# Kernel optimization log

Hardware: AMD Instinct MI355X
Metric: run time of the kernel (lower is better)

## Reference

```python
import jax, jax.numpy as jnp
import numpy as np

B, L, D, DIN, A, V, R = 1024, 100, 256, 704, 128, 32000, 129


def setup_inputs() -> dict:
    key = jax.random.key(0)
    ks = jax.random.split(key, 18)
    s = 0.05
    inp = {
        "x": jax.random.normal(ks[0], (B, DIN), jnp.float32),
        "h0": jax.random.normal(ks[1], (B, D), jnp.float32),
        "c0": jax.random.normal(ks[2], (B, D), jnp.float32),
        "src_enc": jax.random.normal(ks[3], (B, L, D), jnp.float32),
        "src_token_ids": jax.random.randint(ks[4], (B, L), 0, V),
        "W_ih": jax.random.normal(ks[5], (4 * D, DIN), jnp.float32) * s,
        "b_ih": jax.random.normal(ks[6], (4 * D,), jnp.float32) * s,
        "W_hh": jax.random.normal(ks[7], (4 * D, D), jnp.float32) * s,
        "b_hh": jax.random.normal(ks[8], (4 * D,), jnp.float32) * s,
        "W_attn": jax.random.normal(ks[9], (D, D), jnp.float32) * s,
        "W_att_vec": jax.random.normal(ks[10], (A * 2, 2 * D), jnp.float32) * s,
        "W_ptr": jax.random.normal(ks[11], (D, D), jnp.float32) * s,
        "rule_emb": jax.random.normal(ks[12], (R, 128), jnp.float32) * s,
        "W_rule_proj": jax.random.normal(ks[13], (D, 128), jnp.float32) * s,
        "prim_emb": jax.random.normal(ks[14], (V, 128), jnp.float32) * s,
        "W_prim_proj": jax.random.normal(ks[15], (D, 128), jnp.float32) * s,
        "w_gen": jax.random.normal(ks[16], (2, D), jnp.float32) * s,
        "b_gen": jax.random.normal(ks[17], (2,), jnp.float32) * s,
    }
    # W_att_vec maps concat(h, ctx) [2D] -> ATT (=256); keep shape (256, 512)
    inp["W_att_vec"] = inp["W_att_vec"][:256]
    return inp


def reference(x, h0, c0, src_enc, src_token_ids, W_ih, b_ih, W_hh, b_hh,
              W_attn, W_att_vec, W_ptr, rule_emb, W_rule_proj,
              prim_emb, W_prim_proj, w_gen, b_gen):
    # --- LSTMCell (torch gate order i, f, g, o) ---
    gates = x @ W_ih.T + b_ih + h0 @ W_hh.T + b_hh          # [B, 4D]
    i, f, g, o = jnp.split(gates, 4, axis=-1)
    i, f, o = jax.nn.sigmoid(i), jax.nn.sigmoid(f), jax.nn.sigmoid(o)
    c = f * c0 + i * jnp.tanh(g)
    h = o * jnp.tanh(c)                                      # [B, D]

    # --- dot-product attention over source encodings ---
    enc_proj = src_enc @ W_attn.T                            # [B, L, D]
    scores = jnp.einsum('bd,bld->bl', h, enc_proj)
    alpha = jax.nn.softmax(scores, axis=-1)
    ctx = jnp.einsum('bl,bld->bd', alpha, src_enc)
    att = jnp.tanh(jnp.concatenate([h, ctx], axis=-1) @ W_att_vec.T)  # [B, 256]

    # --- apply-rule (production) readout ---
    rule_proj = rule_emb @ W_rule_proj.T                     # [R, 256]
    log_p_rule = jax.nn.log_softmax(att @ rule_proj.T, axis=-1)  # [B, R]

    # --- primitive generation readout ---
    prim_proj = prim_emb @ W_prim_proj.T                     # [V, 256]
    p_gen_prim = jax.nn.softmax(att @ prim_proj.T, axis=-1)  # [B, V]

    # --- pointer network copy distribution over source positions ---
    ptr_scores = jnp.einsum('bld,bd->bl', src_enc @ W_ptr.T, att)
    copy_p = jax.nn.softmax(ptr_scores, axis=-1)             # [B, L]

    # --- gen vs copy gate (softmax over 2, per usage in parse()) ---
    gate = jax.nn.softmax(att @ w_gen.T + b_gen, axis=-1)    # [B, 2]

    # --- combined primitive distribution: gen + scattered copy mass ---
    p_prim = gate[:, :1] * p_gen_prim                        # [B, V]
    copy_mass = gate[:, 1:] * copy_p                         # [B, L]
    bidx = jnp.arange(p_prim.shape[0])[:, None]
    p_prim = p_prim.at[bidx, src_token_ids].add(copy_mass)
    return log_p_rule, p_prim, h, c, att
```

## Files before the change

kernel.cpp:

```cpp
#include <hip/hip_runtime.h>
#include <hip/hip_bf16.h>
#include <math.h>

#define NB   1024
#define LL   100
#define DD   256
#define DINN 704
#define VV   32000
#define RR   129
#define KAV  512
#define ROWU 129

typedef float f32x4 __attribute__((ext_vector_type(4)));
typedef float f32x2 __attribute__((ext_vector_type(2)));
typedef short s16x8 __attribute__((ext_vector_type(8)));
typedef unsigned short u16;
typedef unsigned int u32;

__device__ __forceinline__ float sigf(float x) { return 1.0f / (1.0f + __expf(-x)); }

__device__ __forceinline__ u16 f2bf(float f) {
    u32 u = __float_as_uint(f);
    u += 0x7fffu + ((u >> 16) & 1u);
    return (u16)(u >> 16);
}
__device__ __forceinline__ float bf2f(u16 s) {
    return __uint_as_float(((u32)s) << 16);
}

__global__ __launch_bounds__(256, 2) void k_lstm(
    const float* __restrict__ x, const float* __restrict__ h0, const float* __restrict__ c0,
    const float* __restrict__ W_ih, const float* __restrict__ b_ih,
    const float* __restrict__ W_hh, const float* __restrict__ b_hh,
    float* __restrict__ out_h, float* __restrict__ out_c)
{
    __shared__ __align__(16) float As[16][36];
    __shared__ __align__(16) float Bs[16][68];
    __shared__ __align__(16) float gsm[32][68];
    const int t = threadIdx.x;
    const int row0 = blockIdx.x * 32;
    const int dg = blockIdx.y;
    const int tr = t >> 4, tc = t & 15;
    float acc[2][4] = {};

    for (int kt = 0; kt < 60; ++kt) {
        const float* __restrict__ Asrc;
        const float* __restrict__ Bsrc;
        int lda, kb;
        if (kt < 44) { Asrc = x;  Bsrc = W_ih; lda = DINN; kb = kt * 16; }
        else         { Asrc = h0; Bsrc = W_hh; lda = DD;   kb = (kt - 44) * 16; }
        __syncthreads();
#pragma unroll
        for (int p = 0; p < 2; ++p) {
            int e = t + p * 256;
            int r = e >> 4, kk = e & 15;
            As[kk][r] = Asrc[(row0 + r) * lda + kb + kk];
        }
#pragma unroll
        for (int p = 0; p < 4; ++p) {
            int e = t + p * 256;
            int r = e >> 4, kk = e & 15;
            int n = ((r >> 4) << 8) + dg * 16 + (r & 15);
            Bs[kk][r] = Bsrc[n * lda + kb + kk];
        }
        __syncthreads();
#pragma unroll
        for (int kk = 0; kk < 16; ++kk) {
            float a0 = As[kk][tr * 2], a1 = As[kk][tr * 2 + 1];
            f32x4 b = *reinterpret_cast<const f32x4*>(&Bs[kk][tc * 4]);
#pragma unroll
            for (int i = 0; i < 4; ++i) {
                acc[0][i] = fmaf(a0, b[i], acc[0][i]);
                acc[1][i] = fmaf(a1, b[i], acc[1][i]);
            }
        }
    }
    __syncthreads();
#pragma unroll
    for (int j = 0; j < 2; ++j)
#pragma unroll
        for (int i = 0; i < 4; ++i)
            gsm[tr * 2 + j][tc * 4 + i] = acc[j][i];
    __syncthreads();

#pragma unroll
    for (int p = 0; p < 2; ++p) {
        int item = t + p * 256;
        int r = item >> 4, di = item & 15;
        int dcol = dg * 16 + di;
        float iv = gsm[r][di]      + b_ih[dcol]          + b_hh[dcol];
        float fv = gsm[r][16 + di] + b_ih[DD + dcol]     + b_hh[DD + dcol];
        float gv = gsm[r][32 + di] + b_ih[2 * DD + dcol] + b_hh[2 * DD + dcol];
        float ov = gsm[r][48 + di] + b_ih[3 * DD + dcol] + b_hh[3 * DD + dcol];
        float cprev = c0[(row0 + r) * DD + dcol];
        float cc = sigf(fv) * cprev + sigf(iv) * tanhf(gv);
        float hh = sigf(ov) * tanhf(cc);
        out_c[(row0 + r) * DD + dcol] = cc;
        out_h[(row0 + r) * DD + dcol] = hh;
    }
}

__global__ __launch_bounds__(256) void k_conv(
    const float* __restrict__ src, u16* __restrict__ dst,
    const float* __restrict__ rule_emb, const float* __restrict__ W_rule_proj,
    float* __restrict__ rpT)
{
    __shared__ float re_s[128];
    const int bx = blockIdx.x, t = threadIdx.x;

    if (bx < RR && t < 128) re_s[t] = rule_emb[bx * 128 + t];

    int i = (bx * 256 + t) * 8;
    f32x4 a = *reinterpret_cast<const f32x4*>(&src[i]);
    f32x4 b = *reinterpret_cast<const f32x4*>(&src[i + 4]);
    s16x8 r;
    r[0] = (short)f2bf(a[0]); r[1] = (short)f2bf(a[1]);
    r[2] = (short)f2bf(a[2]); r[3] = (short)f2bf(a[3]);
    r[4] = (short)f2bf(b[0]); r[5] = (short)f2bf(b[1]);
    r[6] = (short)f2bf(b[2]); r[7] = (short)f2bf(b[3]);
    *reinterpret_cast<s16x8*>(&dst[i]) = r;

    if (bx < RR) {
        __syncthreads();
        float acc = 0.f;
        const float* __restrict__ wr = &W_rule_proj[t * 128];
#pragma unroll 8
        for (int k = 0; k < 128; k += 4) {
            f32x4 w4 = *reinterpret_cast<const f32x4*>(&wr[k]);
            acc += w4[0] * re_s[k] + w4[1] * re_s[k + 1]
                 + w4[2] * re_s[k + 2] + w4[3] * re_s[k + 3];
        }
        rpT[t * 192 + bx] = acc;
    }
}

__global__ __launch_bounds__(256) void k_hw(
    const float* __restrict__ h, const float* __restrict__ W_attn, float* __restrict__ hW)
{
    __shared__ __align__(16) float As[16][36];
    __shared__ __align__(16) float Bs[16][68];
    const int t = threadIdx.x;
    const int row0 = blockIdx.x * 32;
    const int col0 = blockIdx.y * 64;
    const int tr = t >> 4, tc = t & 15;
    float acc[2][4] = {};
    for (int kt = 0; kt < 16; ++kt) {
        __syncthreads();
#pragma unroll
        for (int p = 0; p < 2; ++p) {
            int e = t + p * 256;
            int r = e >> 4, kk = e & 15;
            As[kk][r] = h[(row0 + r) * DD + kt * 16 + kk];
        }
#pragma unroll
        for (int p = 0; p < 4; ++p) {
            int e = t + p * 256;
            int kk = e >> 6, c = e & 63;
            Bs[kk][c] = W_attn[(kt * 16 + kk) * DD + col0 + c];
        }
        __syncthreads();
#pragma unroll
        for (int kk = 0; kk < 16; ++kk) {
            float a0 = As[kk][tr * 2], a1 = As[kk][tr * 2 + 1];
            f32x4 b = *reinterpret_cast<const f32x4*>(&Bs[kk][tc * 4]);
#pragma unroll
            for (int i = 0; i < 4; ++i) {
                acc[0][i] = fmaf(a0, b[i], acc[0][i]);
                acc[1][i] = fmaf(a1, b[i], acc[1][i]);
            }
        }
    }
#pragma unroll
    for (int j = 0; j < 2; ++j) {
        f32x4 v;
#pragma unroll
        for (int i = 0; i < 4; ++i) v[i] = acc[j][i];
        *reinterpret_cast<f32x4*>(&hW[(row0 + tr * 2 + j) * DD + col0 + tc * 4]) = v;
    }
}

__global__ __launch_bounds__(256, 2) void k_attn2(
    const float* __restrict__ src_enc, const float* __restrict__ hW,
    float* __restrict__ ctx_out)
{
    __shared__ u32 enc_u[LL * ROWU];
    __shared__ __align__(16) float part[4][DD];
    __shared__ __align__(16) float hw_s[DD];
    __shared__ float sc_s[LL];
    __shared__ float al_s[LL];

    const int b = blockIdx.x, t = threadIdx.x;
    const int lane = t & 63, w = t >> 6;
    const float* __restrict__ enc = src_enc + (size_t)b * LL * DD;

    hw_s[t] = hW[b * DD + t];

#pragma unroll
    for (int p = 0; p < 25; ++p) {
        int q = p * 256 + t;
        int l = q >> 6, dq = q & 63;
        f32x4 ev = *reinterpret_cast<const f32x4*>(&enc[l * DD + dq * 4]);
        u32 w0 = (u32)f2bf(ev[0]) | ((u32)f2bf(ev[1]) << 16);
        u32 w1 = (u32)f2bf(ev[2]) | ((u32)f2bf(ev[3]) << 16);
        enc_u[l * ROWU + dq * 2]     = w0;
        enc_u[l * ROWU + dq * 2 + 1] = w1;
    }
    __syncthreads();

    {
        const int sl = ((w >> 1) << 6) + lane;
        float sp = 0.f;
        if (sl < LL) {
            const u32* __restrict__ rp = enc_u + sl * ROWU + ((w & 1) << 6);
            const float* __restrict__ hp = hw_s + ((w & 1) << 7);
#pragma unroll 32
            for (int k = 0; k < 64; ++k) {
                u32 v = rp[k];
                sp = fmaf(bf2f((u16)v),         hp[2 * k],     sp);
                sp = fmaf(bf2f((u16)(v >> 16)), hp[2 * k + 1], sp);
            }
        }
        part[w][lane] = sp;
    }
    __syncthreads();
    if (t < LL) sc_s[t] = part[(t >> 6) << 1][t & 63] + part[((t >> 6) << 1) + 1][t & 63];
    __syncthreads();

    if (w == 0) {
        float v0 = sc_s[lane];
        float v1 = (lane + 64 < LL) ? sc_s[lane + 64] : -1e30f;
        float m = fmaxf(v0, v1);
#pragma unroll
        for (int s = 1; s < 64; s <<= 1) m = fmaxf(m, __shfl_xor(m, s));
        float e0 = __expf(v0 - m);
        float e1 = (lane + 64 < LL) ? __expf(v1 - m) : 0.f;
        float ssum = e0 + e1;
#pragma unroll
        for (int s = 1; s < 64; s <<= 1) ssum += __shfl_xor(ssum, s);
        float inv = 1.f / ssum;
        al_s[lane] = e0 * inv;
        if (lane + 64 < LL) al_s[lane + 64] = e1 * inv;
    }
    __syncthreads();

    {
        const int l0 = w * 25;
        float c0 = 0.f, c1 = 0.f, c2 = 0.f, c3 = 0.f;
#pragma unroll
        for (int li = 0; li < 25; ++li) {
            int l = l0 + li;
            float a = al_s[l];
            u32 v0 = enc_u[l * ROWU + lane * 2];
            u32 v1 = enc_u[l * ROWU + lane * 2 + 1];
            c0 = fmaf(a, bf2f((u16)v0), c0);
            c1 = fmaf(a, bf2f((u16)(v0 >> 16)), c1);
            c2 = fmaf(a, bf2f((u16)v1), c2);
            c3 = fmaf(a, bf2f((u16)(v1 >> 16)), c3);
        }
        f32x4 p; p[0] = c0; p[1] = c1; p[2] = c2; p[3] = c3;
        *reinterpret_cast<f32x4*>(&part[w][lane * 4]) = p;
    }
    __syncthreads();
    ctx_out[b * DD + t] = (part[0][t] + part[1][t]) + (part[2][t] + part[3][t]);
}

__global__ __launch_bounds__(256) void k_att(
    const float* __restrict__ h, const float* __restrict__ ctx,
    const float* __restrict__ W_att_vec, float* __restrict__ att_out)
{
    __shared__ __align__(16) float As[16][36];
    __shared__ __align__(16) float Bs[16][68];
    const int t = threadIdx.x;
    const int row0 = blockIdx.x * 32;
    const int col0 = blockIdx.y * 64;
    const int tr = t >> 4, tc = t & 15;
    float acc[2][4] = {};
    for (int kt = 0; kt < 32; ++kt) {
        const float* __restrict__ Asrc = (kt < 16) ? h : ctx;
        int kb = (kt < 16) ? kt * 16 : (kt - 16) * 16;
        int kg = kt * 16;
        __syncthreads();
#pragma unroll
        for (int p = 0; p < 2; ++p) {
            int e = t + p * 256;
            int r = e >> 4, kk = e & 15;
            As[kk][r] = Asrc[(row0 + r) * DD + kb + kk];
        }
#pragma unroll
        for (int p = 0; p < 4; ++p) {
            int e = t + p * 256;
            int r = e >> 4, kk = e & 15;
            Bs[kk][r] = W_att_vec[(col0 + r) * KAV + kg + kk];
        }
        __syncthreads();
#pragma unroll
        for (int kk = 0; kk < 16; ++kk) {
            float a0 = As[kk][tr * 2], a1 = As[kk][tr * 2 + 1];
            f32x4 b = *reinterpret_cast<const f32x4*>(&Bs[kk][tc * 4]);
#pragma unroll
            for (int i = 0; i < 4; ++i) {
                acc[0][i] = fmaf(a0, b[i], acc[0][i]);
                acc[1][i] = fmaf(a1, b[i], acc[1][i]);
            }
        }
    }
#pragma unroll
    for (int j = 0; j < 2; ++j)
#pragma unroll
        for (int i = 0; i < 4; ++i)
            att_out[(row0 + tr * 2 + j) * DD + col0 + tc * 4 + i] = tanhf(acc[j][i]);
}

__global__ __launch_bounds__(256) void k_ptrproj(
    const float* __restrict__ att, const float* __restrict__ W_ptr,
    const float* __restrict__ W_prim_proj, const float* __restrict__ rpT,
    float* __restrict__ atw, u16* __restrict__ att_bf, float* __restrict__ rl)
{
    __shared__ __align__(16) float As[16][36];
    __shared__ __align__(16) float Bs[16][68];
    const int t = threadIdx.x;
    const int row0 = blockIdx.x * 32;
    const int col0 = blockIdx.y * 64;
    const int tr = t >> 4, tc = t & 15;
    float acc[2][4] = {};
    for (int kt = 0; kt < 16; ++kt) {
        __syncthreads();
#pragma unroll
        for (int p = 0; p < 2; ++p) {
            int e = t + p * 256;
            int r = e >> 4, kk = e & 15;
            As[kk][r] = att[(row0 + r) * DD + kt * 16 + kk];
        }
#pragma unroll
        for (int p = 0; p < 4; ++p) {
            int e = t + p * 256;
            int kk = e >> 6, c = e & 63;
            float bv;
            if (col0 < 256)      bv = W_ptr[(kt * 16 + kk) * DD + col0 + c];
            else if (col0 < 384) bv = W_prim_proj[(kt * 16 + kk) * 128 + (col0 - 256) + c];
            else {
                int rc = col0 - 384 + c;
                bv = (rc < RR) ? rpT[(kt * 16 + kk) * 192 + rc] : 0.f;
            }
            Bs[kk][c] = bv;
        }
        __syncthreads();
#pragma unroll
        for (int kk = 0; kk < 16; ++kk) {
            float a0 = As[kk][tr * 2], a1 = As[kk][tr * 2 + 1];
            f32x4 b = *reinterpret_cast<const f32x4*>(&Bs[kk][tc * 4]);
#pragma unroll
            for (int i = 0; i < 4; ++i) {
                acc[0][i] = fmaf(a0, b[i], acc[0][i]);
                acc[1][i] = fmaf(a1, b[i], acc[1][i]);
            }
        }
    }
    if (col0 < 256) {
#pragma unroll
        for (int j = 0; j < 2; ++j) {
            f32x4 v;
#pragma unroll
            for (int i = 0; i < 4; ++i) v[i] = acc[j][i];
            *reinterpret_cast<f32x4*>(&atw[(row0 + tr * 2 + j) * DD + col0 + tc * 4]) = v;
        }
    } else if (col0 < 384) {
#pragma unroll
        for (int j = 0; j < 2; ++j)
#pragma unroll
            for (int i = 0; i < 4; ++i)
                att_bf[(row0 + tr * 2 + j) * 128 + (col0 - 256) + tc * 4 + i] = f2bf(acc[j][i]);
    } else {
#pragma unroll
        for (int j = 0; j < 2; ++j)
#pragma unroll
            for (int i = 0; i < 4; ++i) {
                int rc = col0 - 384 + tc * 4 + i;
                if (rc < RR) rl[(row0 + tr * 2 + j) * 132 + rc] = acc[j][i];
            }
    }
}

__global__ __launch_bounds__(256) void k_fin(
    const float* __restrict__ rl, const float* __restrict__ att,
    const float* __restrict__ w_gen, const float* __restrict__ b_gen,
    float* __restrict__ log_p_rule, float* __restrict__ gate0_ws,
    float* __restrict__ gate1_ws)
{
    const int w = threadIdx.x >> 6, lane = threadIdx.x & 63;
    const int b = blockIdx.x * 4 + w;

    float v0 = rl[b * 132 + lane];
    float v1 = rl[b * 132 + 64 + lane];
    float v2 = (lane == 0) ? rl[b * 132 + 128] : -1e30f;
    float m = fmaxf(fmaxf(v0, v1), v2);
#pragma unroll
    for (int s = 1; s < 64; s <<= 1) m = fmaxf(m, __shfl_xor(m, s));
    float ssum = __expf(v0 - m) + __expf(v1 - m) + ((lane == 0) ? __expf(v2 - m) : 0.f);
#pragma unroll
    for (int s = 1; s < 64; s <<= 1) ssum += __shfl_xor(ssum, s);
    float ls = m + logf(ssum);
    log_p_rule[b * RR + lane] = v0 - ls;
    log_p_rule[b * RR + 64 + lane] = v1 - ls;
    if (lane == 0) log_p_rule[b * RR + 128] = v2 - ls;

    f32x4 a4 = *reinterpret_cast<const f32x4*>(&att[b * DD + lane * 4]);
    f32x4 g0 = *reinterpret_cast<const f32x4*>(&w_gen[lane * 4]);
    f32x4 g1 = *reinterpret_cast<const f32x4*>(&w_gen[DD + lane * 4]);
    float p0 = a4[0] * g0[0] + a4[1] * g0[1] + a4[2] * g0[2] + a4[3] * g0[3];
    float p1 = a4[0] * g1[0] + a4[1] * g1[1] + a4[2] * g1[2] + a4[3] * g1[3];
#pragma unroll
    for (int s = 1; s < 64; s <<= 1) { p0 += __shfl_xor(p0, s); p1 += __shfl_xor(p1, s); }
    if (lane == 0) {
        float ga = p0 + b_gen[0], gb = p1 + b_gen[1];
        float gm = fmaxf(ga, gb);
        float ea = __expf(ga - gm), eb = __expf(gb - gm);
        gate0_ws[b] = ea / (ea + eb);
        gate1_ws[b] = eb / (ea + eb);
    }
}

__global__ __launch_bounds__(256, 4) void k_ptr2(
    const float* __restrict__ src_enc, const float* __restrict__ atw,
    const float* __restrict__ gate1_ws, float* __restrict__ copy_mass)
{
    __shared__ __align__(16) float aw_s[DD];
    __shared__ float sc_s[LL];
    const int b = blockIdx.x, t = threadIdx.x;
    const int lane = t & 63, w = t >> 6;

    aw_s[t] = atw[b * DD + t];
    __syncthreads();

    if (t < LL) {
        const float* __restrict__ er = src_enc + (size_t)b * LL * DD + t * DD;
        float a0 = 0.f, a1 = 0.f, a2 = 0.f, a3 = 0.f;
#pragma unroll 16
        for (int d = 0; d < 64; ++d) {
            f32x4 ev = *reinterpret_cast<const f32x4*>(&er[d * 4]);
            f32x4 av = *reinterpret_cast<const f32x4*>(&aw_s[d * 4]);
            a0 = fmaf(ev[0], av[0], a0);
            a1 = fmaf(ev[1], av[1], a1);
            a2 = fmaf(ev[2], av[2], a2);
            a3 = fmaf(ev[3], av[3], a3);
        }
        sc_s[t] = (a0 + a1) + (a2 + a3);
    }
    __syncthreads();

    if (w == 0) {
        float gate1 = gate1_ws[b];
        float v0 = sc_s[lane];
        float v1 = (lane + 64 < LL) ? sc_s[lane + 64] : -1e30f;
        float m = fmaxf(v0, v1);
#pragma unroll
        for (int s = 1; s < 64; s <<= 1) m = fmaxf(m, __shfl_xor(m, s));
        float ee0 = __expf(v0 - m);
        float ee1 = (lane + 64 < LL) ? __expf(v1 - m) : 0.f;
        float ssum = ee0 + ee1;
#pragma unroll
        for (int s = 1; s < 64; s <<= 1) ssum += __shfl_xor(ssum, s);
        float inv = 1.f / ssum;
        copy_mass[b * LL + lane] = gate1 * ee0 * inv;
        if (lane + 64 < LL) copy_mass[b * LL + lane + 64] = gate1 * ee1 * inv;
    }
}

template <int PASS>
__global__ __launch_bounds__(256) void k_prim(
    const u16* __restrict__ att_bf, const u16* __restrict__ prim_bf,
    const float* __restrict__ coef, float* __restrict__ stats, float* __restrict__ p_prim)
{
    const int t = threadIdx.x;
    const int lane = t & 63, w = t >> 6;
    const int lm = lane & 15, lq = lane >> 4;
    const int colbase = blockIdx.x * 128 + (w & 1) * 64;
    const int chunk = colbase >> 6;
    const int rowblk = blockIdx.y * 256;

    s16x8 pfr[4][4];
#pragma unroll
    for (int kg = 0; kg < 4; ++kg)
#pragma unroll
        for (int mg = 0; mg < 4; ++mg)
            pfr[kg][mg] = *reinterpret_cast<const s16x8*>(
                &prim_bf[(size_t)(colbase + mg * 16 + lm) * 128 + kg * 32 + lq * 8]);

    for (int it = 0; it < 2; ++it) {
        const int rowbase = rowblk + it * 128 + (w >> 1) * 64;
        f32x4 acc[4][4] = {};
#pragma unroll
        for (int kg = 0; kg < 4; ++kg) {
            s16x8 afr[4];
#pragma unroll
            for (int ng = 0; ng < 4; ++ng)
                afr[ng] = *reinterpret_cast<const s16x8*>(
                    &att_bf[(rowbase + ng * 16 + lm) * 128 + kg * 32 + lq * 8]);
#pragma unroll
            for (int mg = 0; mg < 4; ++mg)
#pragma unroll
                for (int ng = 0; ng < 4; ++ng)
                    acc[mg][ng] = __builtin_amdgcn_mfma_f32_16x16x32_bf16(
                        pfr[kg][mg], afr[ng], acc[mg][ng], 0, 0, 0);
        }
        if (PASS == 0) {
#pragma unroll
            for (int ng = 0; ng < 4; ++ng) {
                float se = 0.f;
#pragma unroll
                for (int mg = 0; mg < 4; ++mg)
                    se += __expf(acc[mg][ng][0]) + __expf(acc[mg][ng][1])
                        + __expf(acc[mg][ng][2]) + __expf(acc[mg][ng][3]);
                se += __shfl_xor(se, 16);
                se += __shfl_xor(se, 32);
                if (lq == 0)
                    stats[chunk * NB + rowbase + ng * 16 + lm] = se;
            }
        } else {
#pragma unroll
            for (int ng = 0; ng < 4; ++ng) {
                const int arow = rowbase + ng * 16 + lm;
                const float cf = coef[arow];
                float* __restrict__ dst = &p_prim[(size_t)arow * VV + colbase + lq * 4];
#pragma unroll
                for (int mg = 0; mg < 4; ++mg) {
                    f32x4 v;
                    v[0] = cf * __expf(acc[mg][ng][0]);
                    v[1] = cf * __expf(acc[mg][ng][1]);
                    v[2] = cf * __expf(acc[mg][ng][2]);
                    v[3] = cf * __expf(acc[mg][ng][3]);
                    *reinterpret_cast<f32x4*>(&dst[mg * 16]) = v;
                }
            }
        }
    }
}

__global__ __launch_bounds__(256) void k_combine(
    const float* __restrict__ stats, const float* __restrict__ gate0_ws,
    float* __restrict__ coef)
{
    const int row = blockIdx.x * 256 + threadIdx.x;
    float s0 = 0.f, s1 = 0.f, s2 = 0.f, s3 = 0.f;
    for (int c = 0; c < 500; c += 4) {
        s0 += stats[(c)     * NB + row];
        s1 += stats[(c + 1) * NB + row];
        s2 += stats[(c + 2) * NB + row];
        s3 += stats[(c + 3) * NB + row];
    }
    coef[row] = gate0_ws[row] / ((s0 + s1) + (s2 + s3));
}

__global__ __launch_bounds__(256) void k_scatter(
    const int* __restrict__ tok, const float* __restrict__ copy_mass, float* __restrict__ p_prim)
{
    int i = blockIdx.x * 256 + threadIdx.x;
    if (i >= NB * LL) return;
    int b = i / LL;
    atomicAdd(&p_prim[(size_t)b * VV + tok[i]], copy_mass[i]);
}

extern "C" void kernel_launch(void* const* d_in, const int* in_sizes, int n_in,
                              void* d_out, int out_size, void* d_ws, size_t ws_size,
                              hipStream_t stream)
{
    const float* x         = (const float*)d_in[0];
    const float* h0        = (const float*)d_in[1];
    const float* c0        = (const float*)d_in[2];
    const float* src_enc   = (const float*)d_in[3];
    const int*   tok       = (const int*)  d_in[4];
    const float* W_ih      = (const float*)d_in[5];
    const float* b_ih      = (const float*)d_in[6];
    const float* W_hh      = (const float*)d_in[7];
    const float* b_hh      = (const float*)d_in[8];
    const float* W_attn    = (const float*)d_in[9];
    const float* W_att_vec = (const float*)d_in[10];
    const float* W_ptr     = (const float*)d_in[11];
    const float* rule_emb  = (const float*)d_in[12];
    const float* W_rule_pr = (const float*)d_in[13];
    const float* prim_emb  = (const float*)d_in[14];
    const float* W_prim_pr = (const float*)d_in[15];
    const float* w_gen     = (const float*)d_in[16];
    const float* b_gen     = (const float*)d_in[17];

    float* out    = (float*)d_out;
    float* o_logp = out;
    float* o_pp   = out + 1024 * 129;
    float* o_h    = o_pp + (size_t)1024 * 32000;
    float* o_c    = o_h + 1024 * 256;
    float* o_att  = o_c + 1024 * 256;

    float* wsf      = (float*)d_ws;
    float* ws_rpT   = wsf;
    float* ws_rl    = ws_rpT   + 49152;
    float* ws_gate0 = ws_rl    + 135168;
    float* ws_gate1 = ws_gate0 + 1024;
    float* ws_cm    = ws_gate1 + 1024;
    float* ws_coef  = ws_cm    + 102400;
    float* ws_hw    = ws_coef  + 1024;
    float* ws_ctx   = ws_hw    + 262144;
    float* ws_atw   = ws_ctx   + 262144;
    float* ws_stats = ws_atw   + 262144;
    u16*   ws_attbf = (u16*)(ws_stats + 512000);
    u16*   ws_primbf= (u16*)(ws_stats + 512000 + 65536);

    k_conv<<<dim3(2000), 256, 0, stream>>>(prim_emb, ws_primbf, rule_emb, W_rule_pr, ws_rpT);
    k_lstm<<<dim3(32, 16), 256, 0, stream>>>(x, h0, c0, W_ih, b_ih, W_hh, b_hh, o_h, o_c);
    k_hw<<<dim3(32, 4), 256, 0, stream>>>(o_h, W_attn, ws_hw);
    k_attn2<<<dim3(1024), 256, 0, stream>>>(src_enc, ws_hw, ws_ctx);
    k_att<<<dim3(32, 4), 256, 0, stream>>>(o_h, ws_ctx, W_att_vec, o_att);
    k_ptrproj<<<dim3(32, 9), 256, 0, stream>>>(o_att, W_ptr, W_prim_pr, ws_rpT,
                                               ws_atw, ws_attbf, ws_rl);
    k_fin<<<dim3(256), 256, 0, stream>>>(ws_rl, o_att, w_gen, b_gen,
                                         o_logp, ws_gate0, ws_gate1);
    k_ptr2<<<dim3(1024), 256, 0, stream>>>(src_enc, ws_atw, ws_gate1, ws_cm);
    k_prim<0><<<dim3(250, 4), 256, 0, stream>>>(ws_attbf, ws_primbf, nullptr, ws_stats, nullptr);
    k_combine<<<dim3(4), 256, 0, stream>>>(ws_stats, ws_gate0, ws_coef);
    k_prim<1><<<dim3(250, 4), 256, 0, stream>>>(ws_attbf, ws_primbf, ws_coef, nullptr, o_pp);
    k_scatter<<<dim3(400), 256, 0, stream>>>(tok, ws_cm, o_pp);
}
```

Measured before the change: 257.7 us.

## Convert LSTM gate GEMM to bf16 MFMA and warp-reduce pointer scores

The LSTM gate GEMM moves from fp32 FMA tiling with shared memory onto bf16 MFMA 16x16x32 instructions. Fragments are loaded directly from bf16 copies of x, h0, W_ih and W_hh, which the existing conversion kernel now produces as extra blocks. Separately, the pointer-score kernel now computes each dot product with a whole wave and shuffle reduction, replacing one thread per source row, to get coalesced src_enc reads. The price is bf16 precision in the gate pre-activations plus extra conversion traffic and workspace.

```diff
diff --git a/kernel.cpp b/kernel.cpp
--- a/kernel.cpp
+++ b/kernel.cpp
@@ -28,89 +28,28 @@
     return __uint_as_float(((u32)s) << 16);
 }
 
-__global__ __launch_bounds__(256, 2) void k_lstm(
-    const float* __restrict__ x, const float* __restrict__ h0, const float* __restrict__ c0,
-    const float* __restrict__ W_ih, const float* __restrict__ b_ih,
-    const float* __restrict__ W_hh, const float* __restrict__ b_hh,
-    float* __restrict__ out_h, float* __restrict__ out_c)
-{
-    __shared__ __align__(16) float As[16][36];
-    __shared__ __align__(16) float Bs[16][68];
-    __shared__ __align__(16) float gsm[32][68];
-    const int t = threadIdx.x;
-    const int row0 = blockIdx.x * 32;
-    const int dg = blockIdx.y;
-    const int tr = t >> 4, tc = t & 15;
-    float acc[2][4] = {};
-
-    for (int kt = 0; kt < 60; ++kt) {
-        const float* __restrict__ Asrc;
-        const float* __restrict__ Bsrc;
-        int lda, kb;
-        if (kt < 44) { Asrc = x;  Bsrc = W_ih; lda = DINN; kb = kt * 16; }
-        else         { Asrc = h0; Bsrc = W_hh; lda = DD;   kb = (kt - 44) * 16; }
-        __syncthreads();
-#pragma unroll
-        for (int p = 0; p < 2; ++p) {
-            int e = t + p * 256;
-            int r = e >> 4, kk = e & 15;
-            As[kk][r] = Asrc[(row0 + r) * lda + kb + kk];
-        }
-#pragma unroll
-        for (int p = 0; p < 4; ++p) {
-            int e = t + p * 256;
-            int r = e >> 4, kk = e & 15;
-            int n = ((r >> 4) << 8) + dg * 16 + (r & 15);
-            Bs[kk][r] = Bsrc[n * lda + kb + kk];
-        }
-        __syncthreads();
-#pragma unroll
-        for (int kk = 0; kk < 16; ++kk) {
-            float a0 = As[kk][tr * 2], a1 = As[kk][tr * 2 + 1];
-            f32x4 b = *reinterpret_cast<const f32x4*>(&Bs[kk][tc * 4]);
-#pragma unroll
-            for (int i = 0; i < 4; ++i) {
-                acc[0][i] = fmaf(a0, b[i], acc[0][i]);
-                acc[1][i] = fmaf(a1, b[i], acc[1][i]);
-            }
-        }
-    }
-    __syncthreads();
-#pragma unroll
-    for (int j = 0; j < 2; ++j)
-#pragma unroll
-        for (int i = 0; i < 4; ++i)
-            gsm[tr * 2 + j][tc * 4 + i] = acc[j][i];
-    __syncthreads();
-
-#pragma unroll
-    for (int p = 0; p < 2; ++p) {
-        int item = t + p * 256;
-        int r = item >> 4, di = item & 15;
-        int dcol = dg * 16 + di;
-        float iv = gsm[r][di]      + b_ih[dcol]          + b_hh[dcol];
-        float fv = gsm[r][16 + di] + b_ih[DD + dcol]     + b_hh[DD + dcol];
-        float gv = gsm[r][32 + di] + b_ih[2 * DD + dcol] + b_hh[2 * DD + dcol];
-        float ov = gsm[r][48 + di] + b_ih[3 * DD + dcol] + b_hh[3 * DD + dcol];
-        float cprev = c0[(row0 + r) * DD + dcol];
-        float cc = sigf(fv) * cprev + sigf(iv) * tanhf(gv);
-        float hh = sigf(ov) * tanhf(cc);
-        out_c[(row0 + r) * DD + dcol] = cc;
-        out_h[(row0 + r) * DD + dcol] = hh;
-    }
-}
-
 __global__ __launch_bounds__(256) void k_conv(
-    const float* __restrict__ src, u16* __restrict__ dst,
+    const float* __restrict__ prim_emb, u16* __restrict__ prim_bf,
+    const float* __restrict__ W_ih, u16* __restrict__ wih_bf,
+    const float* __restrict__ W_hh, u16* __restrict__ whh_bf,
+    const float* __restrict__ x, u16* __restrict__ x_bf,
+    const float* __restrict__ h0, u16* __restrict__ h0_bf,
     const float* __restrict__ rule_emb, const float* __restrict__ W_rule_proj,
     float* __restrict__ rpT)
 {
     __shared__ float re_s[128];
     const int bx = blockIdx.x, t = threadIdx.x;
 
+    const float* src; u16* dst; int off;
+    if (bx < 2000)      { src = prim_emb; dst = prim_bf; off = bx * 2048; }
+    else if (bx < 2352) { src = W_ih;  dst = wih_bf; off = (bx - 2000) * 2048; }
+    else if (bx < 2480) { src = W_hh;  dst = whh_bf; off = (bx - 2352) * 2048; }
+    else if (bx < 2832) { src = x;     dst = x_bf;   off = (bx - 2480) * 2048; }
+    else                { src = h0;    dst = h0_bf;  off = (bx - 2832) * 2048; }
+
     if (bx < RR && t < 128) re_s[t] = rule_emb[bx * 128 + t];
 
-    int i = (bx * 256 + t) * 8;
+    int i = off + t * 8;
     f32x4 a = *reinterpret_cast<const f32x4*>(&src[i]);
     f32x4 b = *reinterpret_cast<const f32x4*>(&src[i + 4]);
     s16x8 r;
@@ -131,6 +70,86 @@
                  + w4[2] * re_s[k + 2] + w4[3] * re_s[k + 3];
         }
         rpT[t * 192 + bx] = acc;
+    }
+}
+
+__global__ __launch_bounds__(256) void k_lstm(
+    const u16* __restrict__ x_bf, const u16* __restrict__ h0_bf,
+    const float* __restrict__ c0,
+    const u16* __restrict__ wih_bf, const u16* __restrict__ whh_bf,
+    const float* __restrict__ b_ih, const float* __restrict__ b_hh,
+    float* __restrict__ out_h, float* __restrict__ out_c)
+{
+    const int t = threadIdx.x;
+    const int lane = t & 63, w = t >> 6;
+    const int lm = lane & 15, lq = lane >> 4;
+    const int dg = blockIdx.x;
+    const int row0 = blockIdx.y * 128 + w * 32;
+    f32x4 acc[4][2] = {};
+
+    for (int kt = 0; kt < 22; ++kt) {
+        const int ko = kt * 32 + lq * 8;
+        s16x8 bfr[4], afr[2];
+#pragma unroll
+        for (int mg = 0; mg < 4; ++mg)
+            bfr[mg] = *reinterpret_cast<const s16x8*>(
+                &wih_bf[(mg * 256 + dg * 16 + lm) * DINN + ko]);
+#pragma unroll
+        for (int ng = 0; ng < 2; ++ng)
+            afr[ng] = *reinterpret_cast<const s16x8*>(
+                &x_bf[(row0 + ng * 16 + lm) * DINN + ko]);
+#pragma unroll
+        for (int mg = 0; mg < 4; ++mg)
+#pragma unroll
+            for (int ng = 0; ng < 2; ++ng)
+                acc[mg][ng] = __builtin_amdgcn_mfma_f32_16x16x32_bf16(
+                    bfr[mg], afr[ng], acc[mg][ng], 0, 0, 0);
+    }
+    for (int kt = 0; kt < 8; ++kt) {
+        const int ko = kt * 32 + lq * 8;
+        s16x8 bfr[4], afr[2];
+#pragma unroll
+        for (int mg = 0; mg < 4; ++mg)
+            bfr[mg] = *reinterpret_cast<const s16x8*>(
+                &whh_bf[(mg * 256 + dg * 16 + lm) * DD + ko]);
+#pragma unroll
+        for (int ng = 0; ng < 2; ++ng)
+            afr[ng] = *reinterpret_cast<const s16x8*>(
+                &h0_bf[(row0 + ng * 16 + lm) * DD + ko]);
+#pragma unroll
+        for (int mg = 0; mg < 4; ++mg)
+#pragma unroll
+            for (int ng = 0; ng < 2; ++ng)
+                acc[mg][ng] = __builtin_amdgcn_mfma_f32_16x16x32_bf16(
+                    bfr[mg], afr[ng], acc[mg][ng], 0, 0, 0);
+    }
+
+    const int dc = dg * 16 + lq * 4;
+    f32x4 bi[4];
+#pragma unroll
+    for (int mg = 0; mg < 4; ++mg) {
+        f32x4 a4 = *reinterpret_cast<const f32x4*>(&b_ih[mg * 256 + dc]);
+        f32x4 b4 = *reinterpret_cast<const f32x4*>(&b_hh[mg * 256 + dc]);
+        bi[mg][0] = a4[0] + b4[0]; bi[mg][1] = a4[1] + b4[1];
+        bi[mg][2] = a4[2] + b4[2]; bi[mg][3] = a4[3] + b4[3];
+    }
+#pragma unroll
+    for (int ng = 0; ng < 2; ++ng) {
+        const int row = row0 + ng * 16 + lm;
+        f32x4 c4 = *reinterpret_cast<const f32x4*>(&c0[row * DD + dc]);
+        f32x4 h4, cc4;
+#pragma unroll
+        for (int r = 0; r < 4; ++r) {
+            float iv = acc[0][ng][r] + bi[0][r];
+            float fv = acc[1][ng][r] + bi[1][r];
+            float gv = acc[2][ng][r] + bi[2][r];
+            float ov = acc[3][ng][r] + bi[3][r];
+            float cc = sigf(fv) * c4[r] + sigf(iv) * tanhf(gv);
+            cc4[r] = cc;
+            h4[r] = sigf(ov) * tanhf(cc);
+        }
+        *reinterpret_cast<f32x4*>(&out_c[row * DD + dc]) = cc4;
+        *reinterpret_cast<f32x4*>(&out_h[row * DD + dc]) = h4;
     }
 }
 
@@ -420,34 +439,24 @@
     }
 }
 
-__global__ __launch_bounds__(256, 4) void k_ptr2(
+__global__ __launch_bounds__(256) void k_ptr2(
     const float* __restrict__ src_enc, const float* __restrict__ atw,
     const float* __restrict__ gate1_ws, float* __restrict__ copy_mass)
 {
-    __shared__ __align__(16) float aw_s[DD];
     __shared__ float sc_s[LL];
     const int b = blockIdx.x, t = threadIdx.x;
     const int lane = t & 63, w = t >> 6;
-
-    aw_s[t] = atw[b * DD + t];
+    const float* __restrict__ enc = src_enc + (size_t)b * LL * DD;
+    f32x4 aw4 = *reinterpret_cast<const f32x4*>(&atw[b * DD + lane * 4]);
+
+    for (int l = w; l < LL; l += 4) {
+        f32x4 ev = *reinterpret_cast<const f32x4*>(&enc[l * DD + lane * 4]);
+        float pr = aw4[0] * ev[0] + aw4[1] * ev[1] + aw4[2] * ev[2] + aw4[3] * ev[3];
+#pragma unroll
+        for (int m = 1; m < 64; m <<= 1) pr += __shfl_xor(pr, m);
+        if (lane == 0) sc_s[l] = pr;
+    }
     __syncthreads();
-
-    if (t < LL) {
-        const float* __restrict__ er = src_enc + (size_t)b * LL * DD + t * DD;
-        float a0 = 0.f, a1 = 0.f, a2 = 0.f, a3 = 0.f;
-#pragma unroll 16
-        for (int d = 0; d < 64; ++d) {
-            f32x4 ev = *reinterpret_cast<const f32x4*>(&er[d * 4]);
-            f32x4 av = *reinterpret_cast<const f32x4*>(&aw_s[d * 4]);
-            a0 = fmaf(ev[0], av[0], a0);
-            a1 = fmaf(ev[1], av[1], a1);
-            a2 = fmaf(ev[2], av[2], a2);
-            a3 = fmaf(ev[3], av[3], a3);
-        }
-        sc_s[t] = (a0 + a1) + (a2 + a3);
-    }
-    __syncthreads();
-
     if (w == 0) {
         float gate1 = gate1_ws[b];
         float v0 = sc_s[lane];
@@ -601,11 +610,19 @@
     float* ws_ctx   = ws_hw    + 262144;
     float* ws_atw   = ws_ctx   + 262144;
     float* ws_stats = ws_atw   + 262144;
-    u16*   ws_attbf = (u16*)(ws_stats + 512000);
-    u16*   ws_primbf= (u16*)(ws_stats + 512000 + 65536);
-
-    k_conv<<<dim3(2000), 256, 0, stream>>>(prim_emb, ws_primbf, rule_emb, W_rule_pr, ws_rpT);
-    k_lstm<<<dim3(32, 16), 256, 0, stream>>>(x, h0, c0, W_ih, b_ih, W_hh, b_hh, o_h, o_c);
+    u16*   ub       = (u16*)(ws_stats + 512000);
+    u16*   ws_attbf = ub;
+    u16*   ws_primbf= ws_attbf + 131072;
+    u16*   ws_xb    = ws_primbf + 4096000;
+    u16*   ws_h0b   = ws_xb    + 720896;
+    u16*   ws_wihb  = ws_h0b   + 262144;
+    u16*   ws_whhb  = ws_wihb  + 720896;
+
+    k_conv<<<dim3(2960), 256, 0, stream>>>(prim_emb, ws_primbf, W_ih, ws_wihb,
+                                           W_hh, ws_whhb, x, ws_xb, h0, ws_h0b,
+                                           rule_emb, W_rule_pr, ws_rpT);
+    k_lstm<<<dim3(16, 8), 256, 0, stream>>>(ws_xb, ws_h0b, c0, ws_wihb, ws_whhb,
+                                            b_ih, b_hh, o_h, o_c);
     k_hw<<<dim3(32, 4), 256, 0, stream>>>(o_h, W_attn, ws_hw);
     k_attn2<<<dim3(1024), 256, 0, stream>>>(src_enc, ws_hw, ws_ctx);
     k_att<<<dim3(32, 4), 256, 0, stream>>>(o_h, ws_ctx, W_att_vec, o_att);
```

New measurement: 235.0 us. 8.8% less time.
